# Kernel tuning notes

Measured on AMD Instinct MI355X. Metric: run time of the kernel, lower is better.

The kernel has to match this reference:

```python
import jax, jax.numpy as jnp
import numpy as np

EMBED_DIM = 1024
NUM_HEADS = 16
HEAD_DIM = EMBED_DIM // NUM_HEADS


def setup_inputs() -> dict:
    key = jax.random.key(0)
    ks = jax.random.split(key, 9)
    B, N, C = 4, 2048, EMBED_DIM
    scale = 1.0 / np.sqrt(C)
    x = jax.random.normal(ks[0], (B, N, C), dtype=jnp.float32)
    Wq = jax.random.normal(ks[1], (C, C), dtype=jnp.float32) * scale
    bq = jax.random.normal(ks[2], (C,), dtype=jnp.float32) * 0.01
    Wk = jax.random.normal(ks[3], (C, C), dtype=jnp.float32) * scale
    bk = jax.random.normal(ks[4], (C,), dtype=jnp.float32) * 0.01
    Wv = jax.random.normal(ks[5], (C, C), dtype=jnp.float32) * scale
    bv = jax.random.normal(ks[6], (C,), dtype=jnp.float32) * 0.01
    Wo = jax.random.normal(ks[7], (C, C), dtype=jnp.float32) * scale
    bo = jax.random.normal(ks[8], (C,), dtype=jnp.float32) * 0.01
    return {"x": x, "Wq": Wq, "bq": bq, "Wk": Wk, "bk": bk,
            "Wv": Wv, "bv": bv, "Wo": Wo, "bo": bo}


def reference(x, Wq, bq, Wk, bk, Wv, bv, Wo, bo):
    B, N, C = x.shape
    H, D = NUM_HEADS, HEAD_DIM
    # linear projections (weights stored as [in, out])
    Q = (x @ Wq + bq).reshape(B, N, H, D).transpose(0, 2, 1, 3)  # [B,H,N,D]
    K = (x @ Wk + bk).reshape(B, N, H, D).transpose(0, 2, 1, 3)
    V = (x @ Wv + bv).reshape(B, N, H, D).transpose(0, 2, 1, 3)
    scores = jnp.einsum('bhqd,bhkd->bhqk', Q, K) / jnp.sqrt(jnp.float32(D))
    attn = jax.nn.softmax(scores, axis=-1)
    out = jnp.einsum('bhqk,bhkd->bhqd', attn, V)  # [B,H,N,D]
    out = out.transpose(0, 2, 1, 3).reshape(B, N, C)
    return out @ Wo + bo
```

## Files before the change

kernel.cpp:

```cpp
#include <hip/hip_runtime.h>
#include <hip/hip_bf16.h>
#include <cstdint>


typedef __attribute__((ext_vector_type(8))) short short8;
typedef __attribute__((ext_vector_type(4))) float floatx4;

#if __has_builtin(__builtin_amdgcn_exp2f)
#define EXP2F(x) __builtin_amdgcn_exp2f(x)
#else
#define EXP2F(x) __expf((x) * 0.6931471805599453f)
#endif

__device__ __forceinline__ unsigned short f2bf(float f) {
  unsigned u = __float_as_uint(f);
  unsigned r = u + 0x7fffu + ((u >> 16) & 1u);
  return (unsigned short)(r >> 16);
}

__device__ __forceinline__ void async16(const void* g, void* l) {
  __builtin_amdgcn_global_load_lds(
      (__attribute__((address_space(1))) void*)(void*)(uintptr_t)g,
      (__attribute__((address_space(3))) void*)l, 16, 0, 0);
}

__global__ __launch_bounds__(256) void cvt_kernel(const float* __restrict__ in,
                                                  unsigned short* __restrict__ out) {
  int i = (blockIdx.x * 256 + threadIdx.x) * 4;
  float4 v = *(const float4*)(in + i);
  ushort4 o;
  o.x = f2bf(v.x); o.y = f2bf(v.y); o.z = f2bf(v.z); o.w = f2bf(v.w);
  *(ushort4*)(out + i) = o;
}

__global__ __launch_bounds__(256) void trans_w(
    const float* __restrict__ W0, const float* __restrict__ W1,
    const float* __restrict__ W2, const float* __restrict__ W3,
    unsigned short* __restrict__ T0, unsigned short* __restrict__ T1,
    unsigned short* __restrict__ T2, unsigned short* __restrict__ T3) {
  const float* W = blockIdx.z == 0 ? W0 : blockIdx.z == 1 ? W1 : blockIdx.z == 2 ? W2 : W3;
  unsigned short* T = blockIdx.z == 0 ? T0 : blockIdx.z == 1 ? T1 : blockIdx.z == 2 ? T2 : T3;
  __shared__ float t[32][33];
  int tx = threadIdx.x, ty = threadIdx.y;
  int bx = blockIdx.x * 32, by = blockIdx.y * 32;
#pragma unroll
  for (int i = 0; i < 4; ++i)
    t[ty + i * 8][tx] = W[(size_t)(by + ty + i * 8) * 1024 + bx + tx];
  __syncthreads();
#pragma unroll
  for (int i = 0; i < 4; ++i)
    T[(size_t)(bx + ty + i * 8) * 1024 + by + tx] = f2bf(t[tx][ty + i * 8]);
}

__global__ __launch_bounds__(256) void gemm_qkv(
    const unsigned short* __restrict__ A, const unsigned short* __restrict__ BT,
    const float* __restrict__ bq, const float* __restrict__ bk,
    const float* __restrict__ bv,
    unsigned short* __restrict__ Qo, unsigned short* __restrict__ Ko,
    unsigned short* __restrict__ Vo) {
  constexpr int Kd = 1024;
  __shared__ unsigned short sm[8192];
  unsigned short* As = sm;
  unsigned short* Bs = sm + 4096;
  const int tid = threadIdx.x;
  const int wave = tid >> 6, lane = tid & 63;
  const int quad = lane >> 4, l16 = lane & 15;
  const int wm = (wave & 1) * 64, wn = (wave >> 1) * 64;
  const int m0 = blockIdx.x * 128, n0 = blockIdx.y * 128;
  const int mid = blockIdx.y >> 3;
  const float* bias = mid == 0 ? bq : mid == 1 ? bk : bv;
  const float scale = mid == 0 ? 0.180336880021082f : 1.0f;

  floatx4 acc[4][4] = {};
  const unsigned short* Ag = A + (size_t)m0 * Kd;
  const unsigned short* Bg = BT + (size_t)n0 * Kd;

  for (int k0 = 0; k0 < Kd; k0 += 32) {
    __syncthreads();
#pragma unroll
    for (int p = 0; p < 2; ++p) {
      int c = wave * 128 + p * 64 + lane;
      int row = c >> 2, kp = (c & 3) * 8;
      async16(Ag + (size_t)row * Kd + k0 + kp, (char*)As + (size_t)(wave * 128 + p * 64) * 16);
      async16(Bg + (size_t)row * Kd + k0 + kp, (char*)Bs + (size_t)(wave * 128 + p * 64) * 16);
    }
    __syncthreads();
    short8 a[4], b[4];
#pragma unroll
    for (int i = 0; i < 4; ++i) {
      a[i] = *(const short8*)(As + (wm + i * 16 + l16) * 32 + quad * 8);
      b[i] = *(const short8*)(Bs + (wn + i * 16 + l16) * 32 + quad * 8);
    }
#pragma unroll
    for (int i = 0; i < 4; ++i)
#pragma unroll
      for (int j = 0; j < 4; ++j)
        acc[i][j] = __builtin_amdgcn_mfma_f32_16x16x32_bf16(a[i], b[j], acc[i][j], 0, 0, 0);
  }

  const int b = m0 >> 11;
  const int ni0 = m0 & 2047;
#pragma unroll
  for (int p = 0; p < 2; ++p) {
    __syncthreads();
    if ((wave >> 1) == p) {
#pragma unroll
      for (int j = 0; j < 4; ++j) {
        int d = j * 16 + l16;
        int cn = (n0 & 1023) + p * 64 + d;
        float bb = bias[cn];
#pragma unroll
        for (int i = 0; i < 4; ++i) {
#pragma unroll
          for (int r = 0; r < 4; ++r) {
            unsigned short hv = f2bf((acc[i][j][r] + bb) * scale);
            int off;
            if (mid == 2)
              off = (((wm >> 5) + (i >> 1)) * 4 + j) * 512 + quad * 128 + l16 * 8 + r * 2 + (i & 1);
            else
              off = (((wm >> 4) + i) * 2 + (d >> 5)) * 512 + ((d & 31) >> 3) * 128 + (quad * 4 + r) * 8 + (l16 & 7);
            sm[off] = hv;
          }
        }
      }
    }
    __syncthreads();
    int h = ((n0 & 1023) + p * 64) >> 6;
    size_t bh = (size_t)b * 16 + h;
    unsigned short* dstbase;
    if (mid == 2) dstbase = Vo + ((bh * 64 + (ni0 >> 5)) * 4) * 512;
    else dstbase = (mid ? Ko : Qo) + ((bh * 128 + (ni0 >> 4)) * 2) * 512;
#pragma unroll
    for (int it = 0; it < 4; ++it) {
      int c = it * 256 + tid;
      *(short8*)(dstbase + c * 8) = *(const short8*)(sm + c * 8);
    }
  }
}

__global__ __launch_bounds__(256) void attn_kernel(
    const unsigned short* __restrict__ Qs, const unsigned short* __restrict__ Ksw,
    const unsigned short* __restrict__ Vsw, unsigned short* __restrict__ O) {
  __shared__ __align__(16) char smem[17664];

  const int tid = threadIdx.x, wave = tid >> 6, lane = tid & 63;
  const int quad = lane >> 4, l16 = lane & 15;
  const int wk = wave & 1, wqi = wave >> 1;
  int blk = blockIdx.x;
  int xcd = blk & 7, slot = blk >> 3;
  int bh = (slot & 7) * 8 + xcd, qb = slot >> 3;

  unsigned short* Pw = (unsigned short*)smem + wave * 1280;

  short8 aq[2][2];
#pragma unroll
  for (int rt = 0; rt < 2; ++rt)
#pragma unroll
    for (int kk = 0; kk < 2; ++kk)
      aq[rt][kk] = *(const short8*)(Qs +
          (((size_t)bh * 128 + qb * 4 + wqi * 2 + rt) * 2 + kk) * 512 + lane * 8);

  short8 ones;
#pragma unroll
  for (int i = 0; i < 8; ++i) ones[i] = (short)0x3F80;

  const float MSUB = 17.3123404906675611f;
  floatx4 mneg;
#pragma unroll
  for (int i = 0; i < 4; ++i) mneg[i] = -MSUB;

  floatx4 acc_o[2][4] = {};
  floatx4 acc_l[2] = {};

  const unsigned short* kptr = Ksw + (size_t)bh * 128 * 2 * 512 + (size_t)wk * 32 * 2048;
  const unsigned short* vptr = Vsw + (size_t)bh * 64 * 4 * 512 + (size_t)wk * 32 * 2048;

  for (int kti = 0; kti < 32; ++kti) {
    short8 kf[2][2];
#pragma unroll
    for (int ct = 0; ct < 2; ++ct)
#pragma unroll
      for (int kk = 0; kk < 2; ++kk)
        kf[ct][kk] = *(const short8*)(kptr + (ct * 2 + kk) * 512 + lane * 8);
    short8 vf[4];
#pragma unroll
    for (int nt = 0; nt < 4; ++nt)
      vf[nt] = *(const short8*)(vptr + nt * 512 + lane * 8);
    kptr += 2048; vptr += 2048;

    floatx4 sacc[2][2];
#pragma unroll
    for (int rt = 0; rt < 2; ++rt)
#pragma unroll
      for (int ct = 0; ct < 2; ++ct) {
        sacc[rt][ct] = __builtin_amdgcn_mfma_f32_16x16x32_bf16(aq[rt][0], kf[ct][0], mneg, 0, 0, 0);
        sacc[rt][ct] = __builtin_amdgcn_mfma_f32_16x16x32_bf16(aq[rt][1], kf[ct][1], sacc[rt][ct], 0, 0, 0);
      }

#pragma unroll
    for (int rt = 0; rt < 2; ++rt)
#pragma unroll
      for (int r = 0; r < 4; ++r) {
        float pe = EXP2F(sacc[rt][0][r]);
        float po = EXP2F(sacc[rt][1][r]);
        unsigned pk = __builtin_amdgcn_perm(__float_as_uint(po), __float_as_uint(pe), 0x07060302u);
        ((unsigned*)(Pw + (rt * 16 + quad * 4 + r) * 40))[l16] = pk;
      }
#pragma unroll
    for (int rt = 0; rt < 2; ++rt) {
      short8 ap = *(const short8*)(Pw + (rt * 16 + l16) * 40 + quad * 8);
      acc_l[rt] = __builtin_amdgcn_mfma_f32_16x16x32_bf16(ap, ones, acc_l[rt], 0, 0, 0);
#pragma unroll
      for (int nt = 0; nt < 4; ++nt)
        acc_o[rt][nt] = __builtin_amdgcn_mfma_f32_16x16x32_bf16(ap, vf[nt], acc_o[rt][nt], 0, 0, 0);
    }
  }

  float* buf = (float*)smem + wqi * 2176;
  float* lbuf = (float*)(smem + 17408);
  __syncthreads();
  if (wk == 1) {
#pragma unroll
    for (int rt = 0; rt < 2; ++rt)
#pragma unroll
      for (int r = 0; r < 4; ++r) {
        int row = rt * 16 + quad * 4 + r;
#pragma unroll
        for (int nt = 0; nt < 4; ++nt)
          buf[row * 68 + nt * 16 + l16] = acc_o[rt][nt][r];
        if (l16 == 0) lbuf[wqi * 32 + row] = acc_l[rt][r];
      }
  }
  __syncthreads();
  if (wk == 0) {
    const int b = bh >> 4, h = bh & 15;
#pragma unroll
    for (int rt = 0; rt < 2; ++rt)
#pragma unroll
      for (int r = 0; r < 4; ++r) {
        int row = rt * 16 + quad * 4 + r;
        float linv = 1.0f / (acc_l[rt][r] + lbuf[wqi * 32 + row]);
        int grow = qb * 64 + wqi * 32 + row;
#pragma unroll
        for (int nt = 0; nt < 4; ++nt) {
          float v = (acc_o[rt][nt][r] + buf[row * 68 + nt * 16 + l16]) * linv;
          O[((size_t)b * 2048 + grow) * 1024 + h * 64 + nt * 16 + l16] = f2bf(v);
        }
      }
  }
}

__global__ __launch_bounds__(256) void gemm_out(
    const unsigned short* __restrict__ A, const unsigned short* __restrict__ BT,
    const float* __restrict__ bias, float* __restrict__ of) {
  constexpr int Kd = 1024;
  __shared__ unsigned short As[128 * 32];
  __shared__ unsigned short Bs[128 * 32];
  const int tid = threadIdx.x;
  const int wave = tid >> 6, lane = tid & 63;
  const int quad = lane >> 4, l16 = lane & 15;
  const int wm = (wave & 1) * 64, wn = (wave >> 1) * 64;
  const int m0 = blockIdx.x * 128, n0 = blockIdx.y * 128;

  floatx4 acc[4][4] = {};
  const unsigned short* Ag = A + (size_t)m0 * Kd;
  const unsigned short* Bg = BT + (size_t)n0 * Kd;

  for (int k0 = 0; k0 < Kd; k0 += 32) {
    __syncthreads();
#pragma unroll
    for (int p = 0; p < 2; ++p) {
      int c = wave * 128 + p * 64 + lane;
      int row = c >> 2, kp = (c & 3) * 8;
      async16(Ag + (size_t)row * Kd + k0 + kp, (char*)As + (size_t)(wave * 128 + p * 64) * 16);
      async16(Bg + (size_t)row * Kd + k0 + kp, (char*)Bs + (size_t)(wave * 128 + p * 64) * 16);
    }
    __syncthreads();
    short8 a[4], b[4];
#pragma unroll
    for (int i = 0; i < 4; ++i) {
      a[i] = *(const short8*)(As + (wm + i * 16 + l16) * 32 + quad * 8);
      b[i] = *(const short8*)(Bs + (wn + i * 16 + l16) * 32 + quad * 8);
    }
#pragma unroll
    for (int i = 0; i < 4; ++i)
#pragma unroll
      for (int j = 0; j < 4; ++j)
        acc[i][j] = __builtin_amdgcn_mfma_f32_16x16x32_bf16(a[i], b[j], acc[i][j], 0, 0, 0);
  }

#pragma unroll
  for (int j = 0; j < 4; ++j) {
    int col = n0 + wn + j * 16 + l16;
    float bb = bias[col];
#pragma unroll
    for (int i = 0; i < 4; ++i) {
      int rbase = m0 + wm + i * 16 + quad * 4;
#pragma unroll
      for (int r = 0; r < 4; ++r)
        of[(size_t)(rbase + r) * 1024 + col] = acc[i][j][r] + bb;
    }
  }
}

extern "C" void kernel_launch(void* const* d_in, const int* in_sizes, int n_in,
                              void* d_out, int out_size, void* d_ws, size_t ws_size,
                              hipStream_t stream) {
  const float* x  = (const float*)d_in[0];
  const float* Wq = (const float*)d_in[1];
  const float* bq = (const float*)d_in[2];
  const float* Wk = (const float*)d_in[3];
  const float* bk = (const float*)d_in[4];
  const float* Wv = (const float*)d_in[5];
  const float* bv = (const float*)d_in[6];
  const float* Wo = (const float*)d_in[7];
  const float* bo = (const float*)d_in[8];

  char* ws = (char*)d_ws;
  unsigned short* xb  = (unsigned short*)(ws);
  unsigned short* wqt = (unsigned short*)(ws + (16u << 20));
  unsigned short* wkt = (unsigned short*)(ws + (18u << 20));
  unsigned short* wvt = (unsigned short*)(ws + (20u << 20));
  unsigned short* wot = (unsigned short*)(ws + (22u << 20));
  unsigned short* Qb  = (unsigned short*)(ws + (24u << 20));
  unsigned short* Kb  = (unsigned short*)(ws + (40u << 20));
  unsigned short* Vtb = (unsigned short*)(ws + (56u << 20));
  unsigned short* Ob  = (unsigned short*)(ws + (72u << 20));

  cvt_kernel<<<dim3(8192), dim3(256), 0, stream>>>(x, xb);
  trans_w<<<dim3(32, 32, 4), dim3(32, 8), 0, stream>>>(Wq, Wk, Wv, Wo, wqt, wkt, wvt, wot);
  gemm_qkv<<<dim3(64, 24), 256, 0, stream>>>(xb, wqt, bq, bk, bv, Qb, Kb, Vtb);
  attn_kernel<<<dim3(2048), 256, 0, stream>>>(Qb, Kb, Vtb, Ob);
  gemm_out<<<dim3(64, 8), 256, 0, stream>>>(Ob, wot, bo, (float*)d_out);
}
```

Baseline: 302.5 us.

## Software-pipeline attention loop with double-buffered P tiles and merge prep kernels

The attention inner loop is software-pipelined: QK^T MFMAs for the next key tile are issued while the PV MFMAs consume the previous tile's probabilities, using two per-wave P buffers in shared memory. V fragments are loaded one iteration ahead. The intent is to hide exp/LDS round-trip latency behind MFMA work. Separately, the input conversion and weight transpose kernels are merged into one launch to save a kernel launch. Shared memory per block grows, and register pressure rises from the extra live fragments.

```diff
diff --git a/kernel.cpp b/kernel.cpp
--- a/kernel.cpp
+++ b/kernel.cpp
@@ -24,32 +24,36 @@
       (__attribute__((address_space(3))) void*)l, 16, 0, 0);
 }
 
-__global__ __launch_bounds__(256) void cvt_kernel(const float* __restrict__ in,
-                                                  unsigned short* __restrict__ out) {
-  int i = (blockIdx.x * 256 + threadIdx.x) * 4;
-  float4 v = *(const float4*)(in + i);
-  ushort4 o;
-  o.x = f2bf(v.x); o.y = f2bf(v.y); o.z = f2bf(v.z); o.w = f2bf(v.w);
-  *(ushort4*)(out + i) = o;
-}
-
-__global__ __launch_bounds__(256) void trans_w(
+__global__ __launch_bounds__(256) void prep_kernel(
+    const float* __restrict__ x, unsigned short* __restrict__ xb,
     const float* __restrict__ W0, const float* __restrict__ W1,
     const float* __restrict__ W2, const float* __restrict__ W3,
     unsigned short* __restrict__ T0, unsigned short* __restrict__ T1,
     unsigned short* __restrict__ T2, unsigned short* __restrict__ T3) {
-  const float* W = blockIdx.z == 0 ? W0 : blockIdx.z == 1 ? W1 : blockIdx.z == 2 ? W2 : W3;
-  unsigned short* T = blockIdx.z == 0 ? T0 : blockIdx.z == 1 ? T1 : blockIdx.z == 2 ? T2 : T3;
-  __shared__ float t[32][33];
-  int tx = threadIdx.x, ty = threadIdx.y;
-  int bx = blockIdx.x * 32, by = blockIdx.y * 32;
-#pragma unroll
-  for (int i = 0; i < 4; ++i)
-    t[ty + i * 8][tx] = W[(size_t)(by + ty + i * 8) * 1024 + bx + tx];
-  __syncthreads();
-#pragma unroll
-  for (int i = 0; i < 4; ++i)
-    T[(size_t)(bx + ty + i * 8) * 1024 + by + tx] = f2bf(t[tx][ty + i * 8]);
+  const int tid = threadIdx.x;
+  int blk = blockIdx.x;
+  if (blk < 8192) {
+    int i = (blk * 256 + tid) * 4;
+    float4 v = *(const float4*)(x + i);
+    ushort4 o;
+    o.x = f2bf(v.x); o.y = f2bf(v.y); o.z = f2bf(v.z); o.w = f2bf(v.w);
+    *(ushort4*)(xb + i) = o;
+  } else {
+    int t = blk - 8192;
+    int z = t >> 10, tile = t & 1023;
+    const float* W = z == 0 ? W0 : z == 1 ? W1 : z == 2 ? W2 : W3;
+    unsigned short* T = z == 0 ? T0 : z == 1 ? T1 : z == 2 ? T2 : T3;
+    __shared__ float tb[32][33];
+    int tx = tid & 31, ty = tid >> 5;
+    int bx = (tile & 31) * 32, by = (tile >> 5) * 32;
+#pragma unroll
+    for (int i = 0; i < 4; ++i)
+      tb[ty + i * 8][tx] = W[(size_t)(by + ty + i * 8) * 1024 + bx + tx];
+    __syncthreads();
+#pragma unroll
+    for (int i = 0; i < 4; ++i)
+      T[(size_t)(bx + ty + i * 8) * 1024 + by + tx] = f2bf(tb[tx][ty + i * 8]);
+  }
 }
 
 __global__ __launch_bounds__(256) void gemm_qkv(
@@ -141,7 +145,7 @@
 __global__ __launch_bounds__(256) void attn_kernel(
     const unsigned short* __restrict__ Qs, const unsigned short* __restrict__ Ksw,
     const unsigned short* __restrict__ Vsw, unsigned short* __restrict__ O) {
-  __shared__ __align__(16) char smem[17664];
+  __shared__ __align__(16) char smem[20480];
 
   const int tid = threadIdx.x, wave = tid >> 6, lane = tid & 63;
   const int quad = lane >> 4, l16 = lane & 15;
@@ -150,7 +154,8 @@
   int xcd = blk & 7, slot = blk >> 3;
   int bh = (slot & 7) * 8 + xcd, qb = slot >> 3;
 
-  unsigned short* Pw = (unsigned short*)smem + wave * 1280;
+  unsigned short* Pw0 = (unsigned short*)(smem + wave * 5120);
+  unsigned short* Pw1 = (unsigned short*)(smem + wave * 5120 + 2560);
 
   short8 aq[2][2];
 #pragma unroll
@@ -175,28 +180,66 @@
   const unsigned short* kptr = Ksw + (size_t)bh * 128 * 2 * 512 + (size_t)wk * 32 * 2048;
   const unsigned short* vptr = Vsw + (size_t)bh * 64 * 4 * 512 + (size_t)wk * 32 * 2048;
 
-  for (int kti = 0; kti < 32; ++kti) {
-    short8 kf[2][2];
+  short8 kf[2][2], vf[4];
+  floatx4 sacc[2][2];
+
+#pragma unroll
+  for (int ct = 0; ct < 2; ++ct)
+#pragma unroll
+    for (int kk = 0; kk < 2; ++kk)
+      kf[ct][kk] = *(const short8*)(kptr + (ct * 2 + kk) * 512 + lane * 8);
+#pragma unroll
+  for (int nt = 0; nt < 4; ++nt)
+    vf[nt] = *(const short8*)(vptr + nt * 512 + lane * 8);
+  kptr += 2048; vptr += 2048;
+#pragma unroll
+  for (int rt = 0; rt < 2; ++rt)
+#pragma unroll
+    for (int ct = 0; ct < 2; ++ct) {
+      sacc[rt][ct] = __builtin_amdgcn_mfma_f32_16x16x32_bf16(aq[rt][0], kf[ct][0], mneg, 0, 0, 0);
+      sacc[rt][ct] = __builtin_amdgcn_mfma_f32_16x16x32_bf16(aq[rt][1], kf[ct][1], sacc[rt][ct], 0, 0, 0);
+    }
+#pragma unroll
+  for (int rt = 0; rt < 2; ++rt)
+#pragma unroll
+    for (int r = 0; r < 4; ++r) {
+      float pe = EXP2F(sacc[rt][0][r]);
+      float po = EXP2F(sacc[rt][1][r]);
+      unsigned pk = __builtin_amdgcn_perm(__float_as_uint(po), __float_as_uint(pe), 0x07060302u);
+      ((unsigned*)(Pw0 + (rt * 16 + quad * 4 + r) * 40))[l16] = pk;
+    }
+
+  for (int kti = 1; kti < 32; ++kti) {
+    unsigned short* Pprev = (kti & 1) ? Pw0 : Pw1;
+    unsigned short* Pcur  = (kti & 1) ? Pw1 : Pw0;
+    short8 kn[2][2];
 #pragma unroll
     for (int ct = 0; ct < 2; ++ct)
 #pragma unroll
       for (int kk = 0; kk < 2; ++kk)
-        kf[ct][kk] = *(const short8*)(kptr + (ct * 2 + kk) * 512 + lane * 8);
-    short8 vf[4];
+        kn[ct][kk] = *(const short8*)(kptr + (ct * 2 + kk) * 512 + lane * 8);
+    short8 ap[2];
+#pragma unroll
+    for (int rt = 0; rt < 2; ++rt)
+      ap[rt] = *(const short8*)(Pprev + (rt * 16 + l16) * 40 + quad * 8);
+#pragma unroll
+    for (int rt = 0; rt < 2; ++rt)
+#pragma unroll
+      for (int ct = 0; ct < 2; ++ct) {
+        sacc[rt][ct] = __builtin_amdgcn_mfma_f32_16x16x32_bf16(aq[rt][0], kn[ct][0], mneg, 0, 0, 0);
+        sacc[rt][ct] = __builtin_amdgcn_mfma_f32_16x16x32_bf16(aq[rt][1], kn[ct][1], sacc[rt][ct], 0, 0, 0);
+      }
+#pragma unroll
+    for (int rt = 0; rt < 2; ++rt) {
+      acc_l[rt] = __builtin_amdgcn_mfma_f32_16x16x32_bf16(ap[rt], ones, acc_l[rt], 0, 0, 0);
+#pragma unroll
+      for (int nt = 0; nt < 4; ++nt)
+        acc_o[rt][nt] = __builtin_amdgcn_mfma_f32_16x16x32_bf16(ap[rt], vf[nt], acc_o[rt][nt], 0, 0, 0);
+    }
 #pragma unroll
     for (int nt = 0; nt < 4; ++nt)
       vf[nt] = *(const short8*)(vptr + nt * 512 + lane * 8);
     kptr += 2048; vptr += 2048;
-
-    floatx4 sacc[2][2];
-#pragma unroll
-    for (int rt = 0; rt < 2; ++rt)
-#pragma unroll
-      for (int ct = 0; ct < 2; ++ct) {
-        sacc[rt][ct] = __builtin_amdgcn_mfma_f32_16x16x32_bf16(aq[rt][0], kf[ct][0], mneg, 0, 0, 0);
-        sacc[rt][ct] = __builtin_amdgcn_mfma_f32_16x16x32_bf16(aq[rt][1], kf[ct][1], sacc[rt][ct], 0, 0, 0);
-      }
-
 #pragma unroll
     for (int rt = 0; rt < 2; ++rt)
 #pragma unroll
@@ -204,16 +247,16 @@
         float pe = EXP2F(sacc[rt][0][r]);
         float po = EXP2F(sacc[rt][1][r]);
         unsigned pk = __builtin_amdgcn_perm(__float_as_uint(po), __float_as_uint(pe), 0x07060302u);
-        ((unsigned*)(Pw + (rt * 16 + quad * 4 + r) * 40))[l16] = pk;
-      }
-#pragma unroll
-    for (int rt = 0; rt < 2; ++rt) {
-      short8 ap = *(const short8*)(Pw + (rt * 16 + l16) * 40 + quad * 8);
-      acc_l[rt] = __builtin_amdgcn_mfma_f32_16x16x32_bf16(ap, ones, acc_l[rt], 0, 0, 0);
-#pragma unroll
-      for (int nt = 0; nt < 4; ++nt)
-        acc_o[rt][nt] = __builtin_amdgcn_mfma_f32_16x16x32_bf16(ap, vf[nt], acc_o[rt][nt], 0, 0, 0);
-    }
+        ((unsigned*)(Pcur + (rt * 16 + quad * 4 + r) * 40))[l16] = pk;
+      }
+  }
+#pragma unroll
+  for (int rt = 0; rt < 2; ++rt) {
+    short8 apf = *(const short8*)(Pw1 + (rt * 16 + l16) * 40 + quad * 8);
+    acc_l[rt] = __builtin_amdgcn_mfma_f32_16x16x32_bf16(apf, ones, acc_l[rt], 0, 0, 0);
+#pragma unroll
+    for (int nt = 0; nt < 4; ++nt)
+      acc_o[rt][nt] = __builtin_amdgcn_mfma_f32_16x16x32_bf16(apf, vf[nt], acc_o[rt][nt], 0, 0, 0);
   }
 
   float* buf = (float*)smem + wqi * 2176;
@@ -327,8 +370,7 @@
   unsigned short* Vtb = (unsigned short*)(ws + (56u << 20));
   unsigned short* Ob  = (unsigned short*)(ws + (72u << 20));
 
-  cvt_kernel<<<dim3(8192), dim3(256), 0, stream>>>(x, xb);
-  trans_w<<<dim3(32, 32, 4), dim3(32, 8), 0, stream>>>(Wq, Wk, Wv, Wo, wqt, wkt, wvt, wot);
+  prep_kernel<<<dim3(12288), 256, 0, stream>>>(x, xb, Wq, Wk, Wv, Wo, wqt, wkt, wvt, wot);
   gemm_qkv<<<dim3(64, 24), 256, 0, stream>>>(xb, wqt, bq, bk, bv, Qb, Kb, Vtb);
   attn_kernel<<<dim3(2048), 256, 0, stream>>>(Qb, Kb, Vtb, Ob);
   gemm_out<<<dim3(64, 8), 256, 0, stream>>>(Ob, wot, bo, (float*)d_out);
```

Result: no change. 303.1 us (+0.2%).
